# Kernel tuning notes

Hardware: AMD Instinct MI355X
Metric: run time of the kernel (lower is better)

The kernel has to match this reference:

```python
import jax, jax.numpy as jnp
import numpy as np
from jax import lax

B, S, D, H = 2, 2048, 1024, 16
DEPTH = D // H  # 64


def _leaky(x):
    # tf.keras.layers.ReLU(negative_slope=0.1)
    return jnp.where(x >= 0, x, 0.1 * x)


def _split_heads(x):
    # [B,S,D] -> [B,H,S,DEPTH]
    return x.reshape(B, S, H, DEPTH).transpose(0, 2, 1, 3)


def setup_inputs() -> dict:
    key = jax.random.key(0)
    ks = jax.random.split(key, 8)
    w = lambda k: 0.02 * jax.random.normal(k, (D, D), dtype=jnp.float32)
    return {
        "q": jax.random.normal(ks[0], (B, S, D), dtype=jnp.float32),
        "k": jax.random.normal(ks[1], (B, S, D), dtype=jnp.float32),
        "v": jax.random.normal(ks[2], (B, S, D), dtype=jnp.float32),
        "query_mask": jnp.ones((B, S, 1), dtype=jnp.float32),
        "key_mask": jnp.ones((B, S, 1), dtype=jnp.float32),
        "value_mask": jnp.ones((B, S, 1), dtype=jnp.float32),
        "Wq": w(ks[3]), "bq": 0.5 * jnp.ones((D,), dtype=jnp.float32),
        "Wk": w(ks[4]), "bk": 0.5 * jnp.ones((D,), dtype=jnp.float32),
        "Wv": w(ks[5]), "bv": jnp.zeros((D,), dtype=jnp.float32),
        "Wo": w(ks[6]), "bo": jnp.zeros((D,), dtype=jnp.float32),
    }


def _causal_linear_attn(qh, kh, vh):
    # qh,kh,vh: [B,H,S,DEPTH]. Sequential recurrence:
    #   S_t = S_{t-1} + k_t v_t^T ; z_t = z_{t-1} + k_t
    #   out_t = (q_t @ S_t) / (q_t . z_t)
    def step(carry, x):
        S_st, z = carry
        qi, ki, vi = x  # each [B,H,DEPTH]
        S_st = S_st + ki[..., :, None] * vi[..., None, :]  # [B,H,DEPTH,DEPTH]
        z = z + ki
        num = jnp.einsum('bhd,bhde->bhe', qi, S_st)
        den = jnp.einsum('bhd,bhd->bh', qi, z)
        return (S_st, z), num / den[..., None]

    init = (jnp.zeros((B, H, DEPTH, DEPTH), dtype=qh.dtype),
            jnp.zeros((B, H, DEPTH), dtype=qh.dtype))
    xs = (jnp.moveaxis(qh, 2, 0), jnp.moveaxis(kh, 2, 0), jnp.moveaxis(vh, 2, 0))
    _, out = lax.scan(step, init, xs)  # [S,B,H,DEPTH]
    return jnp.moveaxis(out, 0, 2)  # [B,H,S,DEPTH]


def reference(q, k, v, query_mask, key_mask, value_mask,
              Wq, bq, Wk, bk, Wv, bv, Wo, bo):
    q = (q * query_mask) @ Wq + bq
    k = (k * key_mask) @ Wk + bk
    v = (v * value_mask) @ Wv + bv
    q = _leaky(q)
    k = _leaky(k)
    qh, kh, vh = _split_heads(q), _split_heads(k), _split_heads(v)
    attn = _causal_linear_attn(qh, kh, vh)  # [B,H,S,DEPTH]
    concat = attn.transpose(0, 2, 1, 3).reshape(B, S, D)
    return concat @ Wo + bo
```

## Files before the change

### kernel.cpp

```cpp
#include <hip/hip_runtime.h>

#define Bx    2
#define Sx    2048
#define Dx    1024
#define Hx    16
#define NCx   (Sx/64)
#define BHx   (Bx*Hx)
#define Mx    (Bx*Sx)

typedef float    f4 __attribute__((ext_vector_type(4)));
typedef _Float16 h8 __attribute__((ext_vector_type(8)));
typedef _Float16 h4 __attribute__((ext_vector_type(4)));

__device__ __forceinline__ void gl2lds16(const _Float16* g, _Float16* l) {
  __builtin_amdgcn_global_load_lds(
      (const __attribute__((address_space(1))) void*)g,
      (__attribute__((address_space(3))) void*)l, 16, 0, 0);
}

__global__ __launch_bounds__(256) void convert_in(
    const float* __restrict__ q, const float* __restrict__ k,
    const float* __restrict__ v, const float* __restrict__ qm,
    const float* __restrict__ km, const float* __restrict__ vm,
    _Float16* __restrict__ qh, _Float16* __restrict__ kh,
    _Float16* __restrict__ vh)
{
  const int z = blockIdx.y;
  const float* x = (z == 0) ? q : (z == 1) ? k : v;
  const float* m = (z == 0) ? qm : (z == 1) ? km : vm;
  _Float16*    o = (z == 0) ? qh : (z == 1) ? kh : vh;
  const int i8 = blockIdx.x * 256 + threadIdx.x;
  const f4 v0 = *(const f4*)(x + (size_t)i8 * 8);
  const f4 v1 = *(const f4*)(x + (size_t)i8 * 8 + 4);
  const float mf = m[i8 >> 7];
  h8 r;
#pragma unroll
  for (int i = 0; i < 4; i++) {
    r[i]     = (_Float16)(v0[i] * mf);
    r[4 + i] = (_Float16)(v1[i] * mf);
  }
  *(h8*)(o + (size_t)i8 * 8) = r;
}

__global__ __launch_bounds__(256) void convert_w(
    const float* __restrict__ W0, const float* __restrict__ W1,
    const float* __restrict__ W2, const float* __restrict__ W3,
    _Float16* __restrict__ T0, _Float16* __restrict__ T1,
    _Float16* __restrict__ T2, _Float16* __restrict__ T3)
{
  const float* W = (blockIdx.z == 0) ? W0 : (blockIdx.z == 1) ? W1 :
                   (blockIdx.z == 2) ? W2 : W3;
  _Float16* T = (blockIdx.z == 0) ? T0 : (blockIdx.z == 1) ? T1 :
                (blockIdx.z == 2) ? T2 : T3;
  __shared__ float Ws[64 * 68];
  const int tx = threadIdx.x & 15, ty = threadIdx.x >> 4;
  const int k0 = blockIdx.y * 64, n0 = blockIdx.x * 64;
#pragma unroll
  for (int i = 0; i < 4; i++) {
    const int r = ty + 16 * i;
    *(f4*)&Ws[r * 68 + tx * 4] = *(const f4*)&W[(size_t)(k0 + r) * Dx + n0 + tx * 4];
  }
  __syncthreads();
#pragma unroll
  for (int i = 0; i < 4; i++) {
    const int n = ty + 16 * i;
    h4 o;
#pragma unroll
    for (int j = 0; j < 4; j++) o[j] = (_Float16)Ws[(tx * 4 + j) * 68 + n];
    *(h4*)&T[(size_t)(n0 + n) * Dx + k0 + tx * 4] = o;
  }
}

struct GArgs {
  const _Float16* A; const _Float16* Bt; const float* bias;
  void* out; int leaky, half_out;
};

template<int BN, int WR, int WC>
__global__ __launch_bounds__(512, 4) void gemm_f16(GArgs g0, GArgs g1, GArgs g2)
{
  constexpr int GX  = Dx / BN;
  constexpr int LGX = (GX == 8) ? 3 : 4;
  const int wgp = blockIdx.x + GX * (blockIdx.y + 32 * blockIdx.z);
  const int nwg = GX * 32 * gridDim.z;
  const int wgl = (wgp & 7) * (nwg >> 3) + (wgp >> 3);
  const int bxx = wgl & (GX - 1);
  const int byy = (wgl >> LGX) & 31;
  const int bzz = wgl >> (LGX + 5);

  const GArgs g = (bzz == 0) ? g0 : (bzz == 1) ? g1 : g2;
  constexpr int FM = 128 / WR / 16;
  constexpr int FN = BN / WC / 16;
  __shared__ _Float16 As[128 * 64];
  __shared__ _Float16 Bs[BN * 64];
  const int tid = threadIdx.x;
  const int m0 = byy * 128, n0 = bxx * BN;
  const int lane = tid & 63, wave = tid >> 6;
  const int lm = lane & 15, qd = lane >> 4;
  const int wr = wave % WR, wc = wave / WR;
  const int wm0 = wr * (128 / WR), wn0 = wc * (BN / WC);
  const int srow = lane >> 3;
  const int sseg = (lane & 7) ^ srow;
  const _Float16* gA = g.A  + (size_t)(m0 + srow) * Dx + sseg * 8;
  const _Float16* gB = g.Bt + (size_t)(n0 + srow) * Dx + sseg * 8;

  f4 acc[FM][FN];
#pragma unroll
  for (int i = 0; i < FM; i++)
#pragma unroll
    for (int j = 0; j < FN; j++) { f4 z = {0.f, 0.f, 0.f, 0.f}; acc[i][j] = z; }

  for (int kt = 0; kt < Dx; kt += 64) {
    __syncthreads();
#pragma unroll
    for (int u = 0; u < 2; u++) {
      const int t = wave * 2 + u;
      gl2lds16(gA + (size_t)(t * 8) * Dx + kt, &As[t * 512]);
    }
#pragma unroll
    for (int u = 0; u < BN / 64; u++) {
      const int t = wave * (BN / 64) + u;
      gl2lds16(gB + (size_t)(t * 8) * Dx + kt, &Bs[t * 512]);
    }
    __syncthreads();
#pragma unroll
    for (int kk = 0; kk < 2; kk++) {
      const int sp = ((kk * 4 + qd) ^ (lm & 7)) * 8;
      h8 af[FM];
#pragma unroll
      for (int i = 0; i < FM; i++)
        af[i] = *(const h8*)&As[(wm0 + i * 16 + lm) * 64 + sp];
#pragma unroll
      for (int j = 0; j < FN; j++) {
        const h8 bf = *(const h8*)&Bs[(wn0 + j * 16 + lm) * 64 + sp];
#pragma unroll
        for (int i = 0; i < FM; i++)
          acc[i][j] = __builtin_amdgcn_mfma_f32_16x16x32_f16(af[i], bf, acc[i][j], 0, 0, 0);
      }
    }
  }

#pragma unroll
  for (int j = 0; j < FN; j++) {
    const int n = n0 + wn0 + j * 16 + lm;
    const float bz = g.bias[n];
#pragma unroll
    for (int i = 0; i < FM; i++) {
      const int mb = m0 + wm0 + i * 16 + qd * 4;
#pragma unroll
      for (int r = 0; r < 4; r++) {
        float v = acc[i][j][r] + bz;
        if (g.leaky) v = (v >= 0.f) ? v : 0.1f * v;
        if (g.half_out) ((_Float16*)g.out)[(size_t)(mb + r) * Dx + n] = (_Float16)v;
        else            ((float*)g.out)[(size_t)(mb + r) * Dx + n] = v;
      }
    }
  }
}

__global__ __launch_bounds__(256) void chunkkv_mfma(
    const _Float16* __restrict__ kp, const _Float16* __restrict__ vp,
    _Float16* __restrict__ ckvh, float* __restrict__ cz)
{
  __shared__ _Float16 Kt[64 * 64];
  __shared__ _Float16 Vt[64 * 64];
  const int blk = blockIdx.x;
  const int c = blk & (NCx - 1);
  const int bh = blk / NCx;
  const int b = bh / Hx, h = bh % Hx;
  const int tid = threadIdx.x;
  const size_t rowbase = ((size_t)(b * Sx + c * 64)) * Dx + h * 64;

#pragma unroll
  for (int p = 0; p < 2; p++) {
    const int f = tid + 256 * p;
    const int s = f >> 3, g8 = f & 7;
    const h8 hk = *(const h8*)&kp[rowbase + (size_t)s * Dx + g8 * 8];
    const h8 hv = *(const h8*)&vp[rowbase + (size_t)s * Dx + g8 * 8];
#pragma unroll
    for (int i = 0; i < 8; i++) {
      const int r = g8 * 8 + i;
      const int a = r * 64 + ((((s >> 3) ^ (r & 7)) ^ ((r >> 3) & 7)) * 8) + (s & 7);
      Kt[a] = hk[i];
      Vt[a] = hv[i];
    }
  }
  __syncthreads();

  const int lane = tid & 63, w = tid >> 6;
  const int lm = lane & 15, qd = lane >> 4;

  h8 av[2];
  {
    const int rv = w * 16 + lm;
    const int xv = (rv & 7) ^ ((rv >> 3) & 7);
#pragma unroll
    for (int kk = 0; kk < 2; kk++)
      av[kk] = *(const h8*)&Vt[rv * 64 + ((((kk << 2) + qd)) ^ xv) * 8];
  }

#pragma unroll
  for (int dt = 0; dt < 4; dt++) {
    const int rk = dt * 16 + lm;
    const int xk = (rk & 7) ^ ((rk >> 3) & 7);
    f4 acc = {0.f, 0.f, 0.f, 0.f};
#pragma unroll
    for (int kk = 0; kk < 2; kk++) {
      const h8 bf = *(const h8*)&Kt[rk * 64 + ((((kk << 2) + qd)) ^ xk) * 8];
      acc = __builtin_amdgcn_mfma_f32_16x16x32_f16(av[kk], bf, acc, 0, 0, 0);
    }
#pragma unroll
    for (int r = 0; r < 4; r++) {
      const int e = w * 16 + qd * 4 + r;
      ckvh[(size_t)blk * 4096 + e * 64 + dt * 16 + lm] = (_Float16)acc[r];
    }
  }

  {
    const int d = tid >> 2, fr = tid & 3;
    const int dx = (d & 7) ^ ((d >> 3) & 7);
    float dp = 0.f;
#pragma unroll
    for (int j = 0; j < 2; j++) {
      const h8 kv = *(const h8*)&Kt[d * 64 + ((fr * 2 + j) ^ dx) * 8];
#pragma unroll
      for (int i = 0; i < 8; i++) dp += (float)kv[i];
    }
    dp += __shfl_xor(dp, 1);
    dp += __shfl_xor(dp, 2);
    if (fr == 0) cz[(size_t)blk * 64 + d] = dp;
  }
}

__global__ __launch_bounds__(256) void prefix_kernel(
    _Float16* __restrict__ ckvh, float* __restrict__ cz)
{
  const int gid = blockIdx.x * 256 + threadIdx.x;
  const int bh = gid >> 12, el = gid & 4095;
  const size_t base = (((size_t)bh * NCx) << 12) + el;
  float vals[NCx];
#pragma unroll
  for (int c = 0; c < NCx; c++)
    vals[c] = (float)ckvh[base + ((size_t)c << 12)];
  float acc = 0.f;
#pragma unroll
  for (int c = 0; c < NCx; c++) { const float t = vals[c]; vals[c] = acc; acc += t; }
#pragma unroll
  for (int c = 0; c < NCx; c++)
    ckvh[base + ((size_t)c << 12)] = (_Float16)vals[c];

  if (gid < BHx * 64) {
    const int zbh = gid >> 6, d = gid & 63;
    const size_t zb = (size_t)zbh * NCx * 64 + d;
    float zv[NCx];
#pragma unroll
    for (int c = 0; c < NCx; c++) zv[c] = cz[zb + (size_t)c * 64];
    float az = 0.f;
#pragma unroll
    for (int c = 0; c < NCx; c++) { const float t = zv[c]; zv[c] = az; az += t; }
#pragma unroll
    for (int c = 0; c < NCx; c++) cz[zb + (size_t)c * 64] = zv[c];
  }
}

__global__ __launch_bounds__(256) void attn_mfma(
    const _Float16* __restrict__ qp, const _Float16* __restrict__ kp,
    const _Float16* __restrict__ vp, const _Float16* __restrict__ ckvh,
    const float* __restrict__ cz, _Float16* __restrict__ concat)
{
  __shared__ _Float16 Qs[64 * 64];
  __shared__ _Float16 Ks[64 * 64];
  __shared__ _Float16 Vt[64 * 64];
  __shared__ _Float16 Sh[64 * 64];
  __shared__ float zs[64];
  __shared__ float den[64];
  const int blk = blockIdx.x;
  const int c = blk & (NCx - 1);
  const int bh = blk / NCx;
  const int b = bh / Hx, h = bh % Hx;
  const int tid = threadIdx.x;
  const int lane = tid & 63, w = tid >> 6;
  const int lm = lane & 15, qd = lane >> 4;
  const int x7 = lm & 7;
  const size_t rowbase = ((size_t)(b * Sx + c * 64)) * Dx + h * 64;

#pragma unroll
  for (int p = 0; p < 2; p++) {
    const int r  = 32 * p + 8 * w + (lane >> 3);
    const int sg = (lane & 7) ^ (r & 7);
    const int lb = (32 * p + 8 * w) * 64;
    gl2lds16(&qp[rowbase + (size_t)r * Dx + sg * 8], &Qs[lb]);
    gl2lds16(&kp[rowbase + (size_t)r * Dx + sg * 8], &Ks[lb]);
    gl2lds16(&ckvh[(size_t)blk * 4096 + r * 64 + sg * 8], &Sh[lb]);
  }
#pragma unroll
  for (int p = 0; p < 2; p++) {
    const int f = tid + 256 * p;
    const int s = f >> 3, g8 = f & 7;
    const h8 hv = *(const h8*)&vp[rowbase + (size_t)s * Dx + g8 * 8];
#pragma unroll
    for (int i = 0; i < 8; i++) {
      const int e = g8 * 8 + i;
      Vt[e * 64 + ((((s >> 3) ^ (e & 7)) ^ ((e >> 3) & 7)) * 8) + (s & 7)] = hv[i];
    }
  }
  if (tid < 64) zs[tid] = cz[(size_t)blk * 64 + tid];
  __syncthreads();

  h8 aq[2];
#pragma unroll
  for (int kk = 0; kk < 2; kk++)
    aq[kk] = *(const h8*)&Qs[(w * 16 + lm) * 64 + (((kk << 2) + qd) ^ x7) * 8];

  f4 pc[4];
#pragma unroll
  for (int st = 0; st < 4; st++) {
    f4 z4 = {0.f, 0.f, 0.f, 0.f}; pc[st] = z4;
#pragma unroll
    for (int kk = 0; kk < 2; kk++) {
      const h8 bf = *(const h8*)&Ks[(st * 16 + lm) * 64 + (((kk << 2) + qd) ^ x7) * 8];
      pc[st] = __builtin_amdgcn_mfma_f32_16x16x32_f16(aq[kk], bf, pc[st], 0, 0, 0);
    }
  }
  float rsum[4] = {0.f, 0.f, 0.f, 0.f};
#pragma unroll
  for (int st = 0; st < 4; st++) {
    const int s = st * 16 + lm;
#pragma unroll
    for (int r = 0; r < 4; r++) {
      const int t = w * 16 + qd * 4 + r;
      float v = pc[st][r];
      v = (s <= t) ? v : 0.f;
      pc[st][r] = v;
      rsum[r] += v;
    }
  }
#pragma unroll
  for (int r = 0; r < 4; r++) {
    rsum[r] += __shfl_xor(rsum[r], 1);
    rsum[r] += __shfl_xor(rsum[r], 2);
    rsum[r] += __shfl_xor(rsum[r], 4);
    rsum[r] += __shfl_xor(rsum[r], 8);
  }
  {
    const int t = tid >> 2, fr = tid & 3;
    float dp = 0.f;
#pragma unroll
    for (int j = 0; j < 2; j++) {
      const int sg = fr * 2 + j;
      const h8 qv = *(const h8*)&Qs[t * 64 + (sg ^ (t & 7)) * 8];
#pragma unroll
      for (int i = 0; i < 8; i++) dp += (float)qv[i] * zs[sg * 8 + i];
    }
    dp += __shfl_xor(dp, 1);
    dp += __shfl_xor(dp, 2);
    if (fr == 0) den[t] = dp;
  }
  __syncthreads();

  _Float16* Pa = Ks;
#pragma unroll
  for (int st = 0; st < 4; st++) {
#pragma unroll
    for (int r = 0; r < 4; r++) {
      const int row = w * 16 + qd * 4 + r;
      Pa[row * 64 + (((st * 2 + (lm >> 3)) ^ (row & 7)) * 8) + (lm & 7)] =
          (_Float16)pc[st][r];
    }
  }
  if (lm == 0) {
#pragma unroll
    for (int r = 0; r < 4; r++) den[w * 16 + qd * 4 + r] += rsum[r];
  }
  __syncthreads();

  h8 ap[2];
#pragma unroll
  for (int kk = 0; kk < 2; kk++)
    ap[kk] = *(const h8*)&Pa[(w * 16 + lm) * 64 + (((kk << 2) + qd) ^ x7) * 8];

  f4 acc[4];
#pragma unroll
  for (int et = 0; et < 4; et++) {
    const int re = et * 16 + lm;
    const int xv = (re & 7) ^ ((re >> 3) & 7);
    f4 z4 = {0.f, 0.f, 0.f, 0.f}; acc[et] = z4;
#pragma unroll
    for (int kk = 0; kk < 2; kk++) {
      const h8 bv = *(const h8*)&Vt[re * 64 + ((((kk << 2) + qd)) ^ xv) * 8];
      acc[et] = __builtin_amdgcn_mfma_f32_16x16x32_f16(ap[kk], bv, acc[et], 0, 0, 0);
    }
#pragma unroll
    for (int kk = 0; kk < 2; kk++) {
      const h8 bs = *(const h8*)&Sh[re * 64 + (((kk << 2) + qd) ^ x7) * 8];
      acc[et] = __builtin_amdgcn_mfma_f32_16x16x32_f16(aq[kk], bs, acc[et], 0, 0, 0);
    }
  }

#pragma unroll
  for (int r = 0; r < 4; r++) {
    const int row = w * 16 + qd * 4 + r;
    const float inv = 1.f / den[row];
    _Float16* orow = &concat[((size_t)(b * Sx + c * 64 + row)) * Dx + h * 64];
#pragma unroll
    for (int et = 0; et < 4; et++)
      orow[et * 16 + lm] = (_Float16)(acc[et][r] * inv);
  }
}

extern "C" void kernel_launch(void* const* d_in, const int* in_sizes, int n_in,
                              void* d_out, int out_size, void* d_ws, size_t ws_size,
                              hipStream_t stream)
{
  const float* q  = (const float*)d_in[0];
  const float* k  = (const float*)d_in[1];
  const float* v  = (const float*)d_in[2];
  const float* qm = (const float*)d_in[3];
  const float* km = (const float*)d_in[4];
  const float* vm = (const float*)d_in[5];
  const float* Wq = (const float*)d_in[6];
  const float* bq = (const float*)d_in[7];
  const float* Wk = (const float*)d_in[8];
  const float* bk = (const float*)d_in[9];
  const float* Wv = (const float*)d_in[10];
  const float* bv = (const float*)d_in[11];
  const float* Wo = (const float*)d_in[12];
  const float* bo = (const float*)d_in[13];
  float* out = (float*)d_out;

  char* ws = (char*)d_ws;
  _Float16* qh  = (_Float16*)(ws);
  _Float16* kh  = (_Float16*)(ws + 8388608);
  _Float16* vh  = (_Float16*)(ws + 16777216);
  _Float16* Wtq = (_Float16*)(ws + 25165824);
  _Float16* Wtk = (_Float16*)(ws + 27262976);
  _Float16* Wtv = (_Float16*)(ws + 29360128);
  _Float16* Wto = (_Float16*)(ws + 31457280);
  _Float16* qp  = (_Float16*)(ws + 33554432);
  _Float16* kp  = (_Float16*)(ws + 41943040);
  _Float16* vp  = (_Float16*)(ws + 50331648);
  float*    cz  = (float*)   (ws + 58720256);
  _Float16* ckvh   = qh;
  _Float16* concat = kh;

  convert_in<<<dim3(2048, 3), 256, 0, stream>>>(q, k, v, qm, km, vm, qh, kh, vh);
  convert_w<<<dim3(16, 16, 4), 256, 0, stream>>>(Wq, Wk, Wv, Wo, Wtq, Wtk, Wtv, Wto);

  GArgs gq = { qh, Wtq, bq, qp, 1, 1 };
  GArgs gk = { kh, Wtk, bk, kp, 1, 1 };
  GArgs gv = { vh, Wtv, bv, vp, 0, 1 };
  gemm_f16<128, 4, 2><<<dim3(Dx / 128, Mx / 128, 3), 512, 0, stream>>>(gq, gk, gv);

  chunkkv_mfma<<<BHx * NCx, 256, 0, stream>>>(kp, vp, ckvh, cz);
  prefix_kernel<<<512, 256, 0, stream>>>(ckvh, cz);
  attn_mfma<<<BHx * NCx, 256, 0, stream>>>(qp, kp, vp, ckvh, cz, concat);

  GArgs go = { concat, Wto, bo, out, 0, 0 };
  gemm_f16<64, 4, 2><<<dim3(Dx / 64, Mx / 128, 1), 512, 0, stream>>>(go, go, go);
}
```

Baseline: 195.4 us.

## Merge input/weight conversion kernels and fold chunk prefix sum into attention

Combines the activation and weight fp16 conversion kernels into one launch, and removes the separate prefix-sum kernel. Each attention block now sums all preceding chunk KV states and z vectors itself. This saves two kernel launches and a read/write pass over the chunk states. In exchange it adds redundant O(c) reads per block, up to 31 chunks of 8KB each, which makes load uneven across blocks. Accumulation now happens in fp32 before a single fp16 rounding, instead of rounding each stored prefix.

Result: slower. 214.5 us (+9.8%).

```diff
diff --git a/kernel.cpp b/kernel.cpp
--- a/kernel.cpp
+++ b/kernel.cpp
@@ -18,56 +18,57 @@
       (__attribute__((address_space(3))) void*)l, 16, 0, 0);
 }
 
-__global__ __launch_bounds__(256) void convert_in(
+__global__ __launch_bounds__(256) void convert_all(
     const float* __restrict__ q, const float* __restrict__ k,
     const float* __restrict__ v, const float* __restrict__ qm,
     const float* __restrict__ km, const float* __restrict__ vm,
     _Float16* __restrict__ qh, _Float16* __restrict__ kh,
-    _Float16* __restrict__ vh)
-{
-  const int z = blockIdx.y;
-  const float* x = (z == 0) ? q : (z == 1) ? k : v;
-  const float* m = (z == 0) ? qm : (z == 1) ? km : vm;
-  _Float16*    o = (z == 0) ? qh : (z == 1) ? kh : vh;
-  const int i8 = blockIdx.x * 256 + threadIdx.x;
-  const f4 v0 = *(const f4*)(x + (size_t)i8 * 8);
-  const f4 v1 = *(const f4*)(x + (size_t)i8 * 8 + 4);
-  const float mf = m[i8 >> 7];
-  h8 r;
-#pragma unroll
-  for (int i = 0; i < 4; i++) {
-    r[i]     = (_Float16)(v0[i] * mf);
-    r[4 + i] = (_Float16)(v1[i] * mf);
-  }
-  *(h8*)(o + (size_t)i8 * 8) = r;
-}
-
-__global__ __launch_bounds__(256) void convert_w(
+    _Float16* __restrict__ vh,
     const float* __restrict__ W0, const float* __restrict__ W1,
     const float* __restrict__ W2, const float* __restrict__ W3,
     _Float16* __restrict__ T0, _Float16* __restrict__ T1,
     _Float16* __restrict__ T2, _Float16* __restrict__ T3)
 {
-  const float* W = (blockIdx.z == 0) ? W0 : (blockIdx.z == 1) ? W1 :
-                   (blockIdx.z == 2) ? W2 : W3;
-  _Float16* T = (blockIdx.z == 0) ? T0 : (blockIdx.z == 1) ? T1 :
-                (blockIdx.z == 2) ? T2 : T3;
-  __shared__ float Ws[64 * 68];
-  const int tx = threadIdx.x & 15, ty = threadIdx.x >> 4;
-  const int k0 = blockIdx.y * 64, n0 = blockIdx.x * 64;
-#pragma unroll
-  for (int i = 0; i < 4; i++) {
-    const int r = ty + 16 * i;
-    *(f4*)&Ws[r * 68 + tx * 4] = *(const f4*)&W[(size_t)(k0 + r) * Dx + n0 + tx * 4];
-  }
-  __syncthreads();
-#pragma unroll
-  for (int i = 0; i < 4; i++) {
-    const int n = ty + 16 * i;
-    h4 o;
-#pragma unroll
-    for (int j = 0; j < 4; j++) o[j] = (_Float16)Ws[(tx * 4 + j) * 68 + n];
-    *(h4*)&T[(size_t)(n0 + n) * Dx + k0 + tx * 4] = o;
+  const int bx = blockIdx.x;
+  if (bx < 6144) {
+    const int z = bx >> 11;
+    const float* x = (z == 0) ? q : (z == 1) ? k : v;
+    const float* m = (z == 0) ? qm : (z == 1) ? km : vm;
+    _Float16*    o = (z == 0) ? qh : (z == 1) ? kh : vh;
+    const int i8 = (bx & 2047) * 256 + threadIdx.x;
+    const f4 v0 = *(const f4*)(x + (size_t)i8 * 8);
+    const f4 v1 = *(const f4*)(x + (size_t)i8 * 8 + 4);
+    const float mf = m[i8 >> 7];
+    h8 r;
+#pragma unroll
+    for (int i = 0; i < 4; i++) {
+      r[i]     = (_Float16)(v0[i] * mf);
+      r[4 + i] = (_Float16)(v1[i] * mf);
+    }
+    *(h8*)(o + (size_t)i8 * 8) = r;
+  } else {
+    const int idx = bx - 6144;
+    const int wz = idx >> 8, rem = idx & 255;
+    const int wy = rem >> 4, wx = rem & 15;
+    const float* W = (wz == 0) ? W0 : (wz == 1) ? W1 : (wz == 2) ? W2 : W3;
+    _Float16* T = (wz == 0) ? T0 : (wz == 1) ? T1 : (wz == 2) ? T2 : T3;
+    __shared__ float Ws[64 * 68];
+    const int tx = threadIdx.x & 15, ty = threadIdx.x >> 4;
+    const int k0 = wy * 64, n0 = wx * 64;
+#pragma unroll
+    for (int i = 0; i < 4; i++) {
+      const int r = ty + 16 * i;
+      *(f4*)&Ws[r * 68 + tx * 4] = *(const f4*)&W[(size_t)(k0 + r) * Dx + n0 + tx * 4];
+    }
+    __syncthreads();
+#pragma unroll
+    for (int i = 0; i < 4; i++) {
+      const int n = ty + 16 * i;
+      h4 o;
+#pragma unroll
+      for (int j = 0; j < 4; j++) o[j] = (_Float16)Ws[(tx * 4 + j) * 68 + n];
+      *(h4*)&T[(size_t)(n0 + n) * Dx + k0 + tx * 4] = o;
+    }
   }
 }
 
@@ -229,37 +230,6 @@
     dp += __shfl_xor(dp, 1);
     dp += __shfl_xor(dp, 2);
     if (fr == 0) cz[(size_t)blk * 64 + d] = dp;
-  }
-}
-
-__global__ __launch_bounds__(256) void prefix_kernel(
-    _Float16* __restrict__ ckvh, float* __restrict__ cz)
-{
-  const int gid = blockIdx.x * 256 + threadIdx.x;
-  const int bh = gid >> 12, el = gid & 4095;
-  const size_t base = (((size_t)bh * NCx) << 12) + el;
-  float vals[NCx];
-#pragma unroll
-  for (int c = 0; c < NCx; c++)
-    vals[c] = (float)ckvh[base + ((size_t)c << 12)];
-  float acc = 0.f;
-#pragma unroll
-  for (int c = 0; c < NCx; c++) { const float t = vals[c]; vals[c] = acc; acc += t; }
-#pragma unroll
-  for (int c = 0; c < NCx; c++)
-    ckvh[base + ((size_t)c << 12)] = (_Float16)vals[c];
-
-  if (gid < BHx * 64) {
-    const int zbh = gid >> 6, d = gid & 63;
-    const size_t zb = (size_t)zbh * NCx * 64 + d;
-    float zv[NCx];
-#pragma unroll
-    for (int c = 0; c < NCx; c++) zv[c] = cz[zb + (size_t)c * 64];
-    float az = 0.f;
-#pragma unroll
-    for (int c = 0; c < NCx; c++) { const float t = zv[c]; zv[c] = az; az += t; }
-#pragma unroll
-    for (int c = 0; c < NCx; c++) cz[zb + (size_t)c * 64] = zv[c];
   }
 }
 
@@ -291,7 +261,22 @@
     const int lb = (32 * p + 8 * w) * 64;
     gl2lds16(&qp[rowbase + (size_t)r * Dx + sg * 8], &Qs[lb]);
     gl2lds16(&kp[rowbase + (size_t)r * Dx + sg * 8], &Ks[lb]);
-    gl2lds16(&ckvh[(size_t)blk * 4096 + r * 64 + sg * 8], &Sh[lb]);
+  }
+#pragma unroll
+  for (int p = 0; p < 2; p++) {
+    const int f = tid + 256 * p;
+    const int r = f >> 3, sg = f & 7;
+    const _Float16* src = ckvh + ((size_t)(bh * NCx)) * 4096 + r * 64 + sg * 8;
+    float a[8] = {0.f, 0.f, 0.f, 0.f, 0.f, 0.f, 0.f, 0.f};
+    for (int j = 0; j < c; j++) {
+      const h8 vv = *(const h8*)(src + (size_t)j * 4096);
+#pragma unroll
+      for (int i = 0; i < 8; i++) a[i] += (float)vv[i];
+    }
+    h8 o;
+#pragma unroll
+    for (int i = 0; i < 8; i++) o[i] = (_Float16)a[i];
+    *(h8*)&Sh[r * 64 + ((sg ^ (r & 7)) * 8)] = o;
   }
 #pragma unroll
   for (int p = 0; p < 2; p++) {
@@ -304,7 +289,12 @@
       Vt[e * 64 + ((((s >> 3) ^ (e & 7)) ^ ((e >> 3) & 7)) * 8) + (s & 7)] = hv[i];
     }
   }
-  if (tid < 64) zs[tid] = cz[(size_t)blk * 64 + tid];
+  if (tid < 64) {
+    const float* czsrc = cz + ((size_t)(bh * NCx)) * 64 + tid;
+    float az = 0.f;
+    for (int j = 0; j < c; j++) az += czsrc[(size_t)j * 64];
+    zs[tid] = az;
+  }
   __syncthreads();
 
   h8 aq[2];
@@ -443,8 +433,8 @@
   _Float16* ckvh   = qh;
   _Float16* concat = kh;
 
-  convert_in<<<dim3(2048, 3), 256, 0, stream>>>(q, k, v, qm, km, vm, qh, kh, vh);
-  convert_w<<<dim3(16, 16, 4), 256, 0, stream>>>(Wq, Wk, Wv, Wo, Wtq, Wtk, Wtv, Wto);
+  convert_all<<<7168, 256, 0, stream>>>(q, k, v, qm, km, vm, qh, kh, vh,
+                                        Wq, Wk, Wv, Wo, Wtq, Wtk, Wtv, Wto);
 
   GArgs gq = { qh, Wtq, bq, qp, 1, 1 };
   GArgs gk = { kh, Wtk, bk, kp, 1, 1 };
@@ -452,7 +442,6 @@
   gemm_f16<128, 4, 2><<<dim3(Dx / 128, Mx / 128, 3), 512, 0, stream>>>(gq, gk, gv);
 
   chunkkv_mfma<<<BHx * NCx, 256, 0, stream>>>(kp, vp, ckvh, cz);
-  prefix_kernel<<<512, 256, 0, stream>>>(ckvh, cz);
   attn_mfma<<<BHx * NCx, 256, 0, stream>>>(qp, kp, vp, ckvh, cz, concat);
 
   GArgs go = { concat, Wto, bo, out, 0, 0 };
```
